# Optimization experiments

Hardware: AMD Instinct MI355X
Metric: run time of the kernel (lower is better)

## Reference

```python
import jax, jax.numpy as jnp
import numpy as np

SR = 16000
WIN_LENGTH = int(round(SR / 1000.0 * 25))   # 400 samples
HOP_LENGTH = int(round(SR / 1000.0 * 10))   # 160 samples
EPSILON = 1e-12


def _hamming_window(n):
    # torch.hamming_window(n, periodic=True): 0.54 - 0.46*cos(2*pi*k/n)
    k = jnp.arange(n, dtype=jnp.float32)
    return 0.54 - 0.46 * jnp.cos(2.0 * jnp.pi * k / n)


def _fit_window(win, n_fft):
    # Replicates the module's pad-to / crop-to n_fft logic (static shapes).
    L = win.shape[0]
    if L < n_fft:
        pad = n_fft - L
        b = pad // 2
        win = jnp.concatenate([jnp.zeros(b, win.dtype), win, jnp.zeros(pad - b, win.dtype)])
    elif L > n_fft:
        c = (L - n_fft) // 2
        win = win[c:c + n_fft]
    return win


def setup_inputs() -> dict:
    key = jax.random.key(0)
    # (batch, time_step, n_fft//2 + 1, 2) real/imag onesided STFT
    x = jax.random.normal(key, (16, 3000, 201, 2), dtype=jnp.float32)
    return {"x": x}


def reference(x):
    B, T, F, _ = x.shape
    n_fft = 2 * (F - 1)                       # onesided=True
    xc = jax.lax.complex(x[..., 0], x[..., 1])
    # torch.irfft(..., normalized=False, onesided=True) == numpy-style irfft
    q = jnp.fft.irfft(xc, n=n_fft, axis=-1).astype(x.dtype)   # [B, T, n_fft]
    win = _fit_window(_hamming_window(WIN_LENGTH), n_fft)
    q = q * win
    est_len = (T - 1) * HOP_LENGTH + n_fft
    # Fused overlap-add via a single scatter-add instead of a per-frame loop.
    idx = jnp.arange(T)[:, None] * HOP_LENGTH + jnp.arange(n_fft)[None, :]  # [T, n_fft]
    istft = jnp.zeros((B, est_len), x.dtype).at[:, idx].add(q)
    sq_win = win * win
    ssw = jnp.zeros((est_len,), x.dtype).at[idx].add(jnp.broadcast_to(sq_win, (T, n_fft)))
    istft = jnp.where(ssw > EPSILON, istft / ssw, istft)
    # center=True: trim n_fft//2 on each side
    istft = istft[:, n_fft // 2: est_len - n_fft // 2]
    return istft
```

## Files before the change

kernel.cpp:

```cpp
#include <hip/hip_runtime.h>
#include <hip/hip_bf16.h>
#include <math.h>

constexpr int BB     = 16;
constexpr int T      = 3000;
constexpr int F      = 201;
constexpr int NFFT   = 400;
constexpr int HOP    = 160;
constexpr int K      = 402;
constexpr int ESTLEN = (T - 1) * HOP + NFFT;
constexpr int OUTLEN = ESTLEN - NFFT;
constexpr float EPS  = 1e-12f;

constexpr int WJ    = 416;
constexpr int WSTEP = WJ * 32;
constexpr int NSTEP = 13;
constexpr int UT    = 96;
constexpr int ARR   = 98;
constexpr int NTHR  = 384;

typedef short bf16x8 __attribute__((ext_vector_type(8)));
typedef float f32x16 __attribute__((ext_vector_type(16)));

__device__ __forceinline__ unsigned short f2bf(float f) {
    unsigned int u = __float_as_uint(f);
    u = (u + 0x7fffu + ((u >> 16) & 1u)) >> 16;
    return (unsigned short)u;
}

__global__ void build_wt(unsigned short* __restrict__ Wg) {
    int idx = blockIdx.x * blockDim.x + threadIdx.x;
    if (idx >= NSTEP * WSTEP) return;
    int ksg = idx / WSTEP;
    int rem = idx - ksg * WSTEP;
    int j  = rem >> 5;
    int kk = rem & 31;
    int op = kk >> 3;
    int i  = kk & 7;
    int ol = op ^ ((j >> 1) & 3);
    int k  = ksg * 32 + ol * 8 + i;
    float v = 0.f;
    if (j < NFFT && k < K) {
        int f = k >> 1;
        bool is_re = (k & 1) == 0;
        float c = (f == 0 || f == F - 1) ? (1.f / 400.f) : (2.f / 400.f);
        int m = (j * f) % NFFT;
        float ang = (float)(2.0 * M_PI * (double)m / 400.0);
        float tw = is_re ? cosf(ang) : -sinf(ang);
        float win = 0.54f - 0.46f * cosf((float)(2.0 * M_PI * (double)j / 400.0));
        v = c * tw * win;
    }
    Wg[idx] = f2bf(v);
}

__global__ void build_rssw(float* __restrict__ rssw) {
    int p = blockIdx.x * blockDim.x + threadIdx.x;
    if (p >= ESTLEN) return;
    int t_hi = p / HOP; if (t_hi > T - 1) t_hi = T - 1;
    int t_lo = (p >= NFFT) ? ((p - NFFT) / HOP + 1) : 0;
    float s = 0.f;
    for (int t = t_lo; t <= t_hi; ++t) {
        int j = p - t * HOP;
        float w = 0.54f - 0.46f * cosf((float)(2.0 * M_PI * (double)j / 400.0));
        s += w * w;
    }
    rssw[p] = (s > EPS) ? 1.f / s : 1.f;
}

__global__ __launch_bounds__(NTHR, 3)
void istft_fused(const float* __restrict__ A, const unsigned short* __restrict__ Wg,
                 const float* __restrict__ rssw, const float* __restrict__ zpage,
                 float* __restrict__ out) {
    __shared__ __align__(16) unsigned short smem[2 * WSTEP + 2 * ARR * 32];
    unsigned short* WsBuf = smem;
    unsigned short* AsBuf = smem + 2 * WSTEP;

    const int tid  = threadIdx.x;
    const int lane = tid & 63;
    const int w    = tid >> 6;
    const int kh   = (w >= 3) ? 1 : 0;
    const int wu   = kh ? (w - 3) : w;
    const int lj   = lane & 31;
    const int lh   = lane >> 5;
    const int b    = blockIdx.y;
    const int u0   = 1 + blockIdx.x * UT;
    const int tbase = u0 - 2;

    f32x16 acc[5];
    #pragma unroll
    for (int mf = 0; mf < 5; ++mf)
        #pragma unroll
        for (int q = 0; q < 16; ++q) acc[mf][q] = 0.f;

    const int r0  = tid >> 2, p0 = tid & 3;
    const int cl0 = p0 ^ ((r0 >> 1) & 3);
    const int t0  = tbase + r0;
    const float* arow0 = (t0 >= 0 && t0 < T) ? A + (size_t)(b * T + t0) * K : zpage;
    const bool has2 = (tid < 8);
    const int r1  = 96 + (tid >> 2), p1 = tid & 3;
    const int cl1 = p1 ^ ((r1 >> 1) & 3);
    const int t1  = tbase + r1;
    const float* arow1 = (t1 >= 0 && t1 < T) ? A + (size_t)(b * T + t1) * K : zpage;

    auto loadA = [&](int k0, bool tail, float4* d) {
        if (!tail) {
            const float* s0 = arow0 + k0 + cl0 * 8;
            d[0] = *reinterpret_cast<const float4*>(s0);
            d[1] = *reinterpret_cast<const float4*>(s0 + 4);
            if (has2) {
                const float* s1 = arow1 + k0 + cl1 * 8;
                d[2] = *reinterpret_cast<const float4*>(s1);
                d[3] = *reinterpret_cast<const float4*>(s1 + 4);
            }
        } else {
            float v0[8], v1[8];
            #pragma unroll
            for (int i = 0; i < 8; ++i) {
                int ka = k0 + cl0 * 8 + i;
                v0[i] = (ka < K) ? arow0[ka] : 0.f;
            }
            d[0] = make_float4(v0[0], v0[1], v0[2], v0[3]);
            d[1] = make_float4(v0[4], v0[5], v0[6], v0[7]);
            if (has2) {
                #pragma unroll
                for (int i = 0; i < 8; ++i) {
                    int ka = k0 + cl1 * 8 + i;
                    v1[i] = (ka < K) ? arow1[ka] : 0.f;
                }
                d[2] = make_float4(v1[0], v1[1], v1[2], v1[3]);
                d[3] = make_float4(v1[4], v1[5], v1[6], v1[7]);
            }
        }
    };

    auto writeA = [&](unsigned short* dst, const float4* d) {
        union { bf16x8 v; __hip_bfloat162 h[4]; } u;
        u.h[0] = __float22bfloat162_rn(make_float2(d[0].x, d[0].y));
        u.h[1] = __float22bfloat162_rn(make_float2(d[0].z, d[0].w));
        u.h[2] = __float22bfloat162_rn(make_float2(d[1].x, d[1].y));
        u.h[3] = __float22bfloat162_rn(make_float2(d[1].z, d[1].w));
        *reinterpret_cast<bf16x8*>(&dst[r0 * 32 + p0 * 8]) = u.v;
        if (has2) {
            union { bf16x8 v; __hip_bfloat162 h[4]; } u2;
            u2.h[0] = __float22bfloat162_rn(make_float2(d[2].x, d[2].y));
            u2.h[1] = __float22bfloat162_rn(make_float2(d[2].z, d[2].w));
            u2.h[2] = __float22bfloat162_rn(make_float2(d[3].x, d[3].y));
            u2.h[3] = __float22bfloat162_rn(make_float2(d[3].z, d[3].w));
            *reinterpret_cast<bf16x8*>(&dst[r1 * 32 + p1 * 8]) = u2.v;
        }
    };

    auto issueW = [&](unsigned short* dst, int ksg) {
        const unsigned short* sb = Wg + (size_t)ksg * WSTEP;
        #pragma unroll
        for (int p = 0; p < 5; ++p) {
            int P = p * NTHR + tid;
            if (P < WJ * 4) {
                __builtin_amdgcn_global_load_lds(
                    (const __attribute__((address_space(1))) void*)(sb + (size_t)P * 8),
                    (__attribute__((address_space(3))) void*)(dst + (p * NTHR + w * 64) * 8),
                    16, 0, 0);
            }
        }
    };

    const int q4  = kh * 2 + lh;
    const int spl = q4 ^ ((lj >> 1) & 3);

    auto compute = [&](int buf) {
        const unsigned short* Wb = WsBuf + buf * WSTEP;
        const unsigned short* Ab = AsBuf + buf * (ARR * 32);
        bf16x8 af[3];
        #pragma unroll
        for (int dt = 0; dt < 3; ++dt) {
            int r  = wu * 32 + lj + 2 - dt;
            int sl = q4 ^ ((r >> 1) & 3);
            af[dt] = *reinterpret_cast<const bf16x8*>(&Ab[r * 32 + sl * 8]);
        }
        #pragma unroll
        for (int dt = 0; dt < 3; ++dt) {
            const int nmf = (dt < 2) ? 5 : 3;
            #pragma unroll
            for (int mf = 0; mf < 5; ++mf) {
                if (mf < nmf) {
                    int j = dt * 160 + mf * 32 + lj;
                    bf16x8 bf = *reinterpret_cast<const bf16x8*>(&Wb[j * 32 + spl * 8]);
                    acc[mf] = __builtin_amdgcn_mfma_f32_32x32x16_bf16(
                        af[dt], bf, acc[mf], 0, 0, 0);
                }
            }
        }
    };

    {
        float4 d[4];
        loadA(0, false, d);
        issueW(WsBuf, 0);
        writeA(AsBuf, d);
        __syncthreads();
    }

    for (int s = 0; s < NSTEP; ++s) {
        const int cur = s & 1, nxt = cur ^ 1;
        const bool dn = (s + 1 < NSTEP);
        float4 d[4];
        if (dn) {
            loadA((s + 1) * 32, (s + 1) == 12, d);
            issueW(WsBuf + nxt * WSTEP, s + 1);
        }
        compute(cur);
        if (dn) writeA(AsBuf + nxt * (ARR * 32), d);
        __syncthreads();
    }

    float* xch = reinterpret_cast<float*>(smem);
    if (kh == 1) {
        #pragma unroll
        for (int mf = 0; mf < 5; ++mf) {
            int base = ((wu * 5 + mf) * 64 + lane) * 16;
            #pragma unroll
            for (int q = 0; q < 4; ++q)
                *reinterpret_cast<float4*>(&xch[base + q * 4]) =
                    make_float4(acc[mf][q * 4], acc[mf][q * 4 + 1],
                                acc[mf][q * 4 + 2], acc[mf][q * 4 + 3]);
        }
    }
    __syncthreads();
    if (kh == 0) {
        #pragma unroll
        for (int mf = 0; mf < 5; ++mf) {
            int base = ((wu * 5 + mf) * 64 + lane) * 16;
            float part[16];
            #pragma unroll
            for (int q = 0; q < 4; ++q) {
                float4 v = *reinterpret_cast<const float4*>(&xch[base + q * 4]);
                part[q * 4] = v.x; part[q * 4 + 1] = v.y;
                part[q * 4 + 2] = v.z; part[q * 4 + 3] = v.w;
            }
            int m = mf * 32 + lj;
            #pragma unroll
            for (int rg = 0; rg < 16; ++rg) {
                int u  = u0 + wu * 32 + (rg & 3) + 8 * (rg >> 2) + 4 * lh;
                int pe = u * HOP + m;
                int po = pe - (NFFT / 2);
                if (po >= 0 && po < OUTLEN)
                    out[(size_t)b * OUTLEN + po] = (acc[mf][rg] + part[rg]) * rssw[pe];
            }
        }
    }
}

extern "C" void kernel_launch(void* const* d_in, const int* in_sizes, int n_in,
                              void* d_out, int out_size, void* d_ws, size_t ws_size,
                              hipStream_t stream) {
    const float* x = (const float*)d_in[0];
    float* out = (float*)d_out;

    char* ws = (char*)d_ws;
    unsigned short* Wg = (unsigned short*)ws;
    float* rssw = (float*)(ws + 346112);
    float* zpage = (float*)(ws + 346112 + 1920960);

    hipMemsetAsync(zpage, 0, 2048, stream);
    {
        int total = NSTEP * WSTEP;
        build_wt<<<(total + 255) / 256, 256, 0, stream>>>(Wg);
    }
    {
        build_rssw<<<(ESTLEN + 255) / 256, 256, 0, stream>>>(rssw);
    }
    {
        dim3 grid((T + UT - 1) / UT, BB);
        istft_fused<<<grid, NTHR, 0, stream>>>(x, Wg, rssw, zpage, out);
    }
}
```

Before: 71.83 us.

## Generate DFT twiddle-window matrix on the fly in LDS instead of loading

Drops the build_wt pre-pass kernel and the global-to-LDS async loads of the precomputed bf16 basis matrix. Each block now computes the windowed cos/sin coefficients with fast __cosf/__sinf intrinsics and writes them straight into LDS at every k-step. This saves one kernel launch and the global and L2 traffic for the weight matrix. In exchange every block repeats the trig work, which adds ALU and SFU load inside the MFMA loop and slightly changes coefficient accuracy.

```diff
diff --git a/kernel.cpp b/kernel.cpp
--- a/kernel.cpp
+++ b/kernel.cpp
@@ -22,36 +22,7 @@
 typedef short bf16x8 __attribute__((ext_vector_type(8)));
 typedef float f32x16 __attribute__((ext_vector_type(16)));
 
-__device__ __forceinline__ unsigned short f2bf(float f) {
-    unsigned int u = __float_as_uint(f);
-    u = (u + 0x7fffu + ((u >> 16) & 1u)) >> 16;
-    return (unsigned short)u;
-}
-
-__global__ void build_wt(unsigned short* __restrict__ Wg) {
-    int idx = blockIdx.x * blockDim.x + threadIdx.x;
-    if (idx >= NSTEP * WSTEP) return;
-    int ksg = idx / WSTEP;
-    int rem = idx - ksg * WSTEP;
-    int j  = rem >> 5;
-    int kk = rem & 31;
-    int op = kk >> 3;
-    int i  = kk & 7;
-    int ol = op ^ ((j >> 1) & 3);
-    int k  = ksg * 32 + ol * 8 + i;
-    float v = 0.f;
-    if (j < NFFT && k < K) {
-        int f = k >> 1;
-        bool is_re = (k & 1) == 0;
-        float c = (f == 0 || f == F - 1) ? (1.f / 400.f) : (2.f / 400.f);
-        int m = (j * f) % NFFT;
-        float ang = (float)(2.0 * M_PI * (double)m / 400.0);
-        float tw = is_re ? cosf(ang) : -sinf(ang);
-        float win = 0.54f - 0.46f * cosf((float)(2.0 * M_PI * (double)j / 400.0));
-        v = c * tw * win;
-    }
-    Wg[idx] = f2bf(v);
-}
+constexpr float TWO_PI = 6.28318530717958647692f;
 
 __global__ void build_rssw(float* __restrict__ rssw) {
     int p = blockIdx.x * blockDim.x + threadIdx.x;
@@ -68,9 +39,8 @@
 }
 
 __global__ __launch_bounds__(NTHR, 3)
-void istft_fused(const float* __restrict__ A, const unsigned short* __restrict__ Wg,
-                 const float* __restrict__ rssw, const float* __restrict__ zpage,
-                 float* __restrict__ out) {
+void istft_fused(const float* __restrict__ A, const float* __restrict__ rssw,
+                 const float* __restrict__ zpage, float* __restrict__ out) {
     __shared__ __align__(16) unsigned short smem[2 * WSTEP + 2 * ARR * 32];
     unsigned short* WsBuf = smem;
     unsigned short* AsBuf = smem + 2 * WSTEP;
@@ -91,6 +61,50 @@
     for (int mf = 0; mf < 5; ++mf)
         #pragma unroll
         for (int q = 0; q < 16; ++q) acc[mf][q] = 0.f;
+
+    float item_jf[5], item_w[5], item_fb[5];
+    int   item_off[5];
+    #pragma unroll
+    for (int it = 0; it < 5; ++it) {
+        int P  = it * NTHR + tid;
+        int Pc = (P < WJ * 4) ? P : 0;
+        int j  = Pc >> 2;
+        int op = Pc & 3;
+        int ol = op ^ ((j >> 1) & 3);
+        item_jf[it] = (float)j;
+        float win = 0.54f - 0.46f * __cosf((float)j * (TWO_PI / 400.0f));
+        item_w[it] = (j < NFFT) ? win * 0.005f : 0.0f;
+        item_fb[it] = (float)(ol * 4);
+        item_off[it] = Pc * 8;
+    }
+
+    auto genW = [&](unsigned short* dst, int s) {
+        const float fs = (float)(s * 16);
+        #pragma unroll
+        for (int it = 0; it < 5; ++it) {
+            if (it < 4 || tid < (WJ * 4 - 4 * NTHR)) {
+                float fb = fs + item_fb[it];
+                float jf = item_jf[it];
+                float wj = item_w[it];
+                union { bf16x8 v; __hip_bfloat162 h[4]; } u;
+                #pragma unroll
+                for (int q = 0; q < 4; ++q) {
+                    float fi = fb + (float)q;
+                    float sc = wj;
+                    if (s == 0)  { if (fi == 0.0f) sc *= 0.5f; }
+                    if (s == 12) { sc = (fi > 200.0f) ? 0.0f
+                                      : ((fi == 200.0f) ? sc * 0.5f : sc); }
+                    float rv  = jf * fi * (1.0f / 400.0f);
+                    float rev = rv - floorf(rv);
+                    float ang = rev * TWO_PI;
+                    float cv  =  __cosf(ang) * sc;
+                    float sv  = -__sinf(ang) * sc;
+                    u.h[q] = __float22bfloat162_rn(make_float2(cv, sv));
+                }
+                *reinterpret_cast<bf16x8*>(&dst[item_off[it]]) = u.v;
+            }
+        }
+    };
 
     const int r0  = tid >> 2, p0 = tid & 3;
     const int cl0 = p0 ^ ((r0 >> 1) & 3);
@@ -150,20 +164,6 @@
         }
     };
 
-    auto issueW = [&](unsigned short* dst, int ksg) {
-        const unsigned short* sb = Wg + (size_t)ksg * WSTEP;
-        #pragma unroll
-        for (int p = 0; p < 5; ++p) {
-            int P = p * NTHR + tid;
-            if (P < WJ * 4) {
-                __builtin_amdgcn_global_load_lds(
-                    (const __attribute__((address_space(1))) void*)(sb + (size_t)P * 8),
-                    (__attribute__((address_space(3))) void*)(dst + (p * NTHR + w * 64) * 8),
-                    16, 0, 0);
-            }
-        }
-    };
-
     const int q4  = kh * 2 + lh;
     const int spl = q4 ^ ((lj >> 1) & 3);
 
@@ -195,7 +195,7 @@
     {
         float4 d[4];
         loadA(0, false, d);
-        issueW(WsBuf, 0);
+        genW(WsBuf, 0);
         writeA(AsBuf, d);
         __syncthreads();
     }
@@ -206,7 +206,7 @@
         float4 d[4];
         if (dn) {
             loadA((s + 1) * 32, (s + 1) == 12, d);
-            issueW(WsBuf + nxt * WSTEP, s + 1);
+            genW(WsBuf + nxt * WSTEP, s + 1);
         }
         compute(cur);
         if (dn) writeA(AsBuf + nxt * (ARR * 32), d);
@@ -257,20 +257,12 @@
     float* out = (float*)d_out;
 
     char* ws = (char*)d_ws;
-    unsigned short* Wg = (unsigned short*)ws;
-    float* rssw = (float*)(ws + 346112);
-    float* zpage = (float*)(ws + 346112 + 1920960);
+    float* rssw  = (float*)ws;
+    float* zpage = (float*)(ws + 1920960);
 
     hipMemsetAsync(zpage, 0, 2048, stream);
-    {
-        int total = NSTEP * WSTEP;
-        build_wt<<<(total + 255) / 256, 256, 0, stream>>>(Wg);
-    }
-    {
-        build_rssw<<<(ESTLEN + 255) / 256, 256, 0, stream>>>(rssw);
-    }
-    {
-        dim3 grid((T + UT - 1) / UT, BB);
-        istft_fused<<<grid, NTHR, 0, stream>>>(x, Wg, rssw, zpage, out);
-    }
+    build_rssw<<<(ESTLEN + 255) / 256, 256, 0, stream>>>(rssw);
+
+    dim3 grid((T + UT - 1) / UT, BB);
+    istft_fused<<<grid, NTHR, 0, stream>>>(x, rssw, zpage, out);
 }
```

New measurement: 95.82 us. +33.4%, slower.
